# Performance work log

Hardware: AMD Instinct MI355X
Metric: run time of the kernel (lower is better)

Reference implementation:

```python
import jax, jax.numpy as jnp
import numpy as np

N = 2048   # num nodes
D = 512    # hidden_dim


def setup_inputs() -> dict:
    key = jax.random.key(0)
    k1, k2 = jax.random.split(key)
    x = jax.random.normal(k1, (N, D), dtype=jnp.float32)
    # linear: hidden_dim -> 1 (xavier-like scale)
    w = jax.random.normal(k2, (D,), dtype=jnp.float32) * (1.0 / np.sqrt(D))
    b = jnp.zeros((1,), dtype=jnp.float32)
    return {"x": x, "w": w, "b": b}


def reference(x, w, b):
    # euclidean_distance_matrix + linear fused:
    # s[i,j] = sum_d w_d * (x[i,d]-x[j,d])^2 + b
    #        = q_i + q_j - 2*(x*w) @ x^T + b,  q_i = sum_d w_d x[i,d]^2
    xw = x * w                              # [N, D]
    q = jnp.sum(xw * x, axis=1)             # [N]
    cross = xw @ x.T                        # [N, N]
    s = q[:, None] + q[None, :] - 2.0 * cross + b[0]
    grouping_matrix = jax.nn.sigmoid(s)     # [N, N]

    # compute_fielder, similarity_graph='base'
    W = grouping_matrix
    degree = jnp.sum(W, axis=1)
    L = jnp.diag(degree) - W                # symmetric graph Laplacian
    eigen_values, eigen_vectors = jnp.linalg.eigh(L)
    order = jnp.argsort(jnp.abs(eigen_values))
    fielder_value = eigen_values[order[1]]
    fielder_vector = eigen_vectors[:, order[1]]
    return grouping_matrix, fielder_value, fielder_vector
```

## Files before the change

kernel.cpp:

```cpp
#include <hip/hip_runtime.h>
#include <math.h>

constexpr int NN = 2048;
constexpr int DD_ = 512;
constexpr int LM = 64;
constexpr int VS = NN + 32;
constexpr int GPART = 8;
#define SIGN_FLIP 1


typedef __attribute__((ext_vector_type(4))) float f32x4;
typedef __attribute__((ext_vector_type(8))) short bf16x8;

__device__ inline double waveReduceSum(double v) {
#pragma unroll
  for (int off = 32; off; off >>= 1) v += __shfl_down(v, off, 64);
  return v;
}

__device__ inline double blockReduceSum256(double v) {
  __shared__ double sm[4];
  int lane = threadIdx.x & 63;
  int wid  = threadIdx.x >> 6;
  v = waveReduceSum(v);
  __syncthreads();
  if (lane == 0) sm[wid] = v;
  __syncthreads();
  double r = 0.0;
  if (threadIdx.x < 4) r = sm[threadIdx.x];
  if (wid == 0) {
    r += __shfl_down(r, 2, 64);
    r += __shfl_down(r, 1, 64);
  }
  return r;
}

__device__ inline double blockReduceSum128(double v) {
  __shared__ double sm[2];
  int lane = threadIdx.x & 63;
  int wid  = threadIdx.x >> 6;
  v = waveReduceSum(v);
  if (lane == 0) sm[wid] = v;
  __syncthreads();
  double r = 0.0;
  if (threadIdx.x == 0) r = sm[0] + sm[1];
  return r;
}

__device__ inline unsigned short f2bf(float f) {
  unsigned u = __float_as_uint(f);
  u += 0x7FFFu + ((u >> 16) & 1u);
  return (unsigned short)(u >> 16);
}
__device__ inline float bf2f(unsigned short h) {
  return __uint_as_float(((unsigned)h) << 16);
}

__global__ __launch_bounds__(128) void k_cvtq(const float* __restrict__ x,
                                              const float* __restrict__ w,
                                              float* __restrict__ q,
                                              unsigned short* __restrict__ ah,
                                              unsigned short* __restrict__ al,
                                              unsigned short* __restrict__ bh,
                                              unsigned short* __restrict__ bl) {
  int row = blockIdx.x, t = threadIdx.x;
  int d = 4 * t;
  float4 xv = *(const float4*)&x[(size_t)row * DD_ + d];
  float4 wv = *(const float4*)&w[d];
  float xs[4] = {xv.x, xv.y, xv.z, xv.w};
  float wsv[4] = {wv.x, wv.y, wv.z, wv.w};
  unsigned short rah[4], ral[4], rbh[4], rbl[4];
  float accq = 0.f;
#pragma unroll
  for (int kq = 0; kq < 4; ++kq) {
    float xf = xs[kq], wf = wsv[kq];
    float a = xf * wf;
    unsigned short h = f2bf(a);
    rah[kq] = h;
    ral[kq] = f2bf(a - bf2f(h));
    unsigned short hb = f2bf(xf);
    rbh[kq] = hb;
    rbl[kq] = f2bf(xf - bf2f(hb));
    accq += wf * xf * xf;
  }
  ushort4 vA = {rah[0], rah[1], rah[2], rah[3]};
  ushort4 vAl = {ral[0], ral[1], ral[2], ral[3]};
  ushort4 vB = {rbh[0], rbh[1], rbh[2], rbh[3]};
  ushort4 vBl = {rbl[0], rbl[1], rbl[2], rbl[3]};
  *(ushort4*)&ah[(size_t)row * DD_ + d] = vA;
  *(ushort4*)&al[(size_t)row * DD_ + d] = vAl;
  *(ushort4*)&bh[(size_t)row * DD_ + d] = vB;
  *(ushort4*)&bl[(size_t)row * DD_ + d] = vBl;
  double rq = blockReduceSum128((double)accq);
  if (t == 0) q[row] = (float)rq;
}

__global__ __launch_bounds__(256) void k_Wm(const unsigned short* __restrict__ ah,
                                            const unsigned short* __restrict__ al,
                                            const unsigned short* __restrict__ bh,
                                            const unsigned short* __restrict__ bl,
                                            const float* __restrict__ q,
                                            const float* __restrict__ bptr,
                                            float* __restrict__ out) {
  __shared__ unsigned short As[2][128][40];
  __shared__ unsigned short Bs[2][128][40];
  const int t = threadIdx.x;
  const int i0 = blockIdx.y * 128, j0 = blockIdx.x * 128;
  const int lane = t & 63, wv = t >> 6;
  const int wr = wv >> 1, wc = wv & 1;
  const int fr = lane & 15, kc = lane >> 4;
  const int srow = t >> 1, scol = (t & 1) * 16;

  f32x4 acc[4][4];
#pragma unroll
  for (int a = 0; a < 4; ++a)
#pragma unroll
    for (int b = 0; b < 4; ++b) acc[a][b] = (f32x4){0.f, 0.f, 0.f, 0.f};

  {
    bf16x8 ra0 = *(const bf16x8*)&ah[(size_t)(i0 + srow) * DD_ + scol];
    bf16x8 ra1 = *(const bf16x8*)&ah[(size_t)(i0 + srow) * DD_ + scol + 8];
    bf16x8 rb0 = *(const bf16x8*)&bh[(size_t)(j0 + srow) * DD_ + scol];
    bf16x8 rb1 = *(const bf16x8*)&bh[(size_t)(j0 + srow) * DD_ + scol + 8];
    *(bf16x8*)&As[0][srow][scol] = ra0;
    *(bf16x8*)&As[0][srow][scol + 8] = ra1;
    *(bf16x8*)&Bs[0][srow][scol] = rb0;
    *(bf16x8*)&Bs[0][srow][scol + 8] = rb1;
  }
  __syncthreads();
  int cur = 0;
  for (int s = 0; s < 48; ++s) {
    bf16x8 na0, na1, nb0, nb1;
    if (s + 1 < 48) {
      int pass = (s + 1) >> 4;
      int kk = ((s + 1) & 15) * 32;
      const unsigned short* srcA = (pass == 2) ? al : ah;
      const unsigned short* srcB = (pass == 1) ? bl : bh;
      na0 = *(const bf16x8*)&srcA[(size_t)(i0 + srow) * DD_ + kk + scol];
      na1 = *(const bf16x8*)&srcA[(size_t)(i0 + srow) * DD_ + kk + scol + 8];
      nb0 = *(const bf16x8*)&srcB[(size_t)(j0 + srow) * DD_ + kk + scol];
      nb1 = *(const bf16x8*)&srcB[(size_t)(j0 + srow) * DD_ + kk + scol + 8];
    }
    bf16x8 af[4], bq[4];
#pragma unroll
    for (int a = 0; a < 4; ++a)
      af[a] = *(const bf16x8*)&As[cur][wr * 64 + a * 16 + fr][kc * 8];
#pragma unroll
    for (int b = 0; b < 4; ++b)
      bq[b] = *(const bf16x8*)&Bs[cur][wc * 64 + b * 16 + fr][kc * 8];
#pragma unroll
    for (int a = 0; a < 4; ++a)
#pragma unroll
      for (int b = 0; b < 4; ++b)
        acc[a][b] = __builtin_amdgcn_mfma_f32_16x16x32_bf16(af[a], bq[b], acc[a][b], 0, 0, 0);
    if (s + 1 < 48) {
      *(bf16x8*)&As[cur ^ 1][srow][scol] = na0;
      *(bf16x8*)&As[cur ^ 1][srow][scol + 8] = na1;
      *(bf16x8*)&Bs[cur ^ 1][srow][scol] = nb0;
      *(bf16x8*)&Bs[cur ^ 1][srow][scol + 8] = nb1;
    }
    __syncthreads();
    cur ^= 1;
  }
  float b0 = bptr[0];
#pragma unroll
  for (int a = 0; a < 4; ++a) {
#pragma unroll
    for (int rg = 0; rg < 4; ++rg) {
      int i = i0 + wr * 64 + a * 16 + kc * 4 + rg;
      float qi = q[i];
#pragma unroll
      for (int b = 0; b < 4; ++b) {
        int j = j0 + wc * 64 + b * 16 + fr;
        float s = qi + q[j] - 2.0f * acc[a][b][rg] + b0;
        out[(size_t)i * NN + j] = 1.0f / (1.0f + expf(-s));
      }
    }
  }
}

__global__ __launch_bounds__(256) void k_init(double* __restrict__ r,
                                              double* __restrict__ part) {
  int t = threadIdx.x;
  double loc[8];
  double s = 0.0;
#pragma unroll
  for (int p = 0; p < 8; ++p) {
    unsigned i = (unsigned)(t + 256 * p);
    unsigned u = i * 2654435761u + 0x9E3779B9u;
    u ^= u >> 16; u *= 0x85EBCA6Bu; u ^= u >> 13; u *= 0xC2B2AE35u; u ^= u >> 16;
    double val = ((double)u / 4294967296.0) - 0.5;
    loc[p] = val; s += val;
  }
  __shared__ double mean_s, inv_s;
  double tot = blockReduceSum256(s);
  if (t == 0) mean_s = tot / (double)NN;
  __syncthreads();
  double mean = mean_s;
  double ss = 0.0;
#pragma unroll
  for (int p = 0; p < 8; ++p) { loc[p] -= mean; ss += loc[p] * loc[p]; }
  double tss = blockReduceSum256(ss);
  if (t == 0) inv_s = 1.0 / sqrt(tss);
  __syncthreads();
  double inv = inv_s;
#pragma unroll
  for (int p = 0; p < 8; ++p) r[t + 256 * p] = loc[p] * inv;
  if (t < GPART) part[t] = (t == 0) ? 1.0 : 0.0;
}

__global__ __launch_bounds__(256) void k_mva(const float* __restrict__ Wm,
                                             double* __restrict__ deg,
                                             const double* __restrict__ rprev,
                                             const double* __restrict__ part,
                                             double* __restrict__ V,
                                             double* __restrict__ wstash,
                                             double* __restrict__ c,
                                             double* __restrict__ beta, int j) {
  int b = blockIdx.x, t = threadIdx.x;
  double ss = 0.0;
#pragma unroll
  for (int p = 0; p < GPART; ++p) ss += part[p];
  double bet = sqrt(ss);
  double inv = (bet > 1e-3) ? 1.0 / bet : 0.0;

  if (b < NN) {
    const float* wr = Wm + (size_t)b * NN;
    double acc = 0.0, dsum = 0.0;
    if (j == 0) {
#pragma unroll
      for (int p = 0; p < 2; ++p) {
        int i = 4 * t + 1024 * p;
        float4 wl = *(const float4*)&wr[i];
        dsum += (double)wl.x + (double)wl.y + (double)wl.z + (double)wl.w;
        acc += (double)wl.x * rprev[i] + (double)wl.y * rprev[i + 1] +
               (double)wl.z * rprev[i + 2] + (double)wl.w * rprev[i + 3];
      }
    } else {
#pragma unroll
      for (int p = 0; p < 2; ++p) {
        int i = 4 * t + 1024 * p;
        float4 wl = *(const float4*)&wr[i];
        acc += (double)wl.x * rprev[i] + (double)wl.y * rprev[i + 1] +
               (double)wl.z * rprev[i + 2] + (double)wl.w * rprev[i + 3];
      }
    }
    double red = blockReduceSum256(acc);
    double dred = 0.0;
    if (j == 0) dred = blockReduceSum256(dsum);
    if (t == 0) {
      double d;
      if (j == 0) { d = dred; deg[b] = d; }
      else d = deg[b];
      double vj = rprev[b] * inv;
      V[(size_t)j * VS + b] = vj;
      wstash[(size_t)j * VS + b] = d * vj - red * inv;
      if (b == 0 && j > 0) beta[j - 1] = (bet > 1e-3) ? bet : 0.0;
    }
  } else {
    int q = b - NN;
    const double* wq = wstash + (size_t)q * VS;
    double a = 0.0;
#pragma unroll
    for (int p = 0; p < 8; ++p) { int i = t + 256 * p; a += wq[i] * rprev[i]; }
    double red = blockReduceSum256(a);
    if (t == 0) c[q] = red * inv;
  }
}

__global__ __launch_bounds__(256) void k_orthb(const double* __restrict__ V,
                                               const double* __restrict__ wstash,
                                               const double* __restrict__ c,
                                               double* __restrict__ r,
                                               double* __restrict__ part,
                                               double* __restrict__ alpha, int j) {
  __shared__ double cs[LM];
  __shared__ double cj_s, s1_s;
  int b = blockIdx.x, t = threadIdx.x;
  const double* wj = wstash + (size_t)j * VS;
  const double* vj = V + (size_t)j * VS;
  double a = 0.0, s = 0.0;
#pragma unroll
  for (int p = 0; p < 8; ++p) {
    int i = t + 256 * p;
    double wv = wj[i];
    a += vj[i] * wv;
    s += wv;
  }
  double cj = blockReduceSum256(a);
  double s1 = blockReduceSum256(s);
  if (t == 0) { cj_s = cj; s1_s = s1; }
  for (int k = t; k < j; k += 256) cs[k] = c[k];
  __syncthreads();
  double cjv = cj_s, s1v = s1_s;
  int i = b * 256 + t;
  double val = wj[i] - s1v / (double)NN - cjv * vj[i];
  for (int k = 0; k < j; ++k) val -= cs[k] * V[(size_t)k * VS + i];
  r[i] = val;
  double rr = blockReduceSum256(val * val);
  if (t == 0) {
    part[b] = rr;
    if (b == 0) alpha[j] = cjv;
  }
}

__device__ inline double guardpiv(double d) {
  if (fabs(d) < 1e-280) return (d < 0.0) ? -1e-280 : 1e-280;
  return d;
}

__global__ __launch_bounds__(64) void k_tri(const double* __restrict__ alpha,
                                            const double* __restrict__ beta,
                                            double* __restrict__ svec) {
  __shared__ double al[LM], be[LM];
  __shared__ double Dg[LM], Dl[LM], Du[LM], Du2[LM], bb[LM];
  __shared__ unsigned char piv[LM];
  __shared__ double bounds[2];
  __shared__ int cnts[64];
  __shared__ int meff_s;
  int t = threadIdx.x;
  for (int i = t; i < LM; i += 64) { al[i] = alpha[i]; be[i] = (i < LM - 1) ? beta[i] : 0.0; }
  __syncthreads();
  if (t == 0) {
    int m = LM;
    for (int i = 0; i < LM; ++i) {
      if (!isfinite(al[i])) { m = i; break; }
      if (i < LM - 1 && (be[i] == 0.0 || !isfinite(be[i]))) { m = i + 1; break; }
    }
    if (m < 2) m = 2;
    meff_s = m;
  }
  __syncthreads();
  const int n = meff_s;
  double lo = 1e300, hi = -1e300;
  for (int i = t; i < n; i += 64) {
    double r = 0.0;
    if (i > 0) r += fabs(be[i - 1]);
    if (i < n - 1) r += fabs(be[i]);
    lo = fmin(lo, al[i] - r);
    hi = fmax(hi, al[i] + r);
  }
#pragma unroll
  for (int off = 32; off; off >>= 1) {
    lo = fmin(lo, __shfl_down(lo, off, 64));
    hi = fmax(hi, __shfl_down(hi, off, 64));
  }
  if (t == 0) { bounds[0] = lo; bounds[1] = hi; }
  __syncthreads();
  for (int round = 0; round < 3; ++round) {
    double L0 = bounds[0], H0 = bounds[1];
    double p = L0 + (H0 - L0) * ((double)(t + 1) / 65.0);
    int cnt = 0;
    double d = al[0] - p;
    if (d < 0) cnt++;
    for (int i = 1; i < n; ++i) {
      if (fabs(d) < 1e-300) d = (d < 0.0) ? -1e-300 : 1e-300;
      double bi = be[i - 1];
      d = (al[i] - p) - bi * bi / d;
      if (d < 0) cnt++;
    }
    cnts[t] = cnt;
    __syncthreads();
    if (t == 0) {
      double nl = L0, nh = H0;
      for (int l = 0; l < 64; ++l) {
        double pl = L0 + (H0 - L0) * ((double)(l + 1) / 65.0);
        if (cnts[l] == 0) nl = pl;
        else { nh = pl; break; }
      }
      bounds[0] = nl; bounds[1] = nh;
    }
    __syncthreads();
  }
  double sigma = 0.5 * (bounds[0] + bounds[1]);
  if (t == 0) {
    for (int i = 0; i < n; ++i) Dg[i] = al[i] - sigma;
    for (int i = 0; i < n - 1; ++i) { Dl[i] = be[i]; Du[i] = be[i]; }
    for (int i = 0; i < n - 2; ++i) Du2[i] = 0.0;
    for (int i = 0; i < n - 1; ++i) {
      if (fabs(Dg[i]) >= fabs(Dl[i])) {
        double dpiv = guardpiv(Dg[i]);
        double fact = Dl[i] / dpiv;
        Dl[i] = fact;
        Dg[i + 1] -= fact * Du[i];
        piv[i] = 0;
      } else {
        double fact = Dg[i] / Dl[i];
        Dg[i] = Dl[i]; Dl[i] = fact;
        double temp = Du[i];
        Du[i] = Dg[i + 1];
        Dg[i + 1] = temp - fact * Dg[i + 1];
        if (i < n - 2) { Du2[i] = Du[i + 1]; Du[i + 1] = -fact * Du[i + 1]; }
        piv[i] = 1;
      }
    }
    for (int i = 0; i < n; ++i) bb[i] = 1.0;
    for (int i = 0; i < n - 1; ++i) {
      if (!piv[i]) bb[i + 1] -= Dl[i] * bb[i];
      else { double tmp = bb[i]; bb[i] = bb[i + 1]; bb[i + 1] = tmp - Dl[i] * bb[i]; }
    }
    bb[n - 1] = bb[n - 1] / guardpiv(Dg[n - 1]);
    bb[n - 2] = (bb[n - 2] - Du[n - 2] * bb[n - 1]) / guardpiv(Dg[n - 2]);
    for (int i = n - 3; i >= 0; --i)
      bb[i] = (bb[i] - Du[i] * bb[i + 1] - Du2[i] * bb[i + 2]) / guardpiv(Dg[i]);
    double nrm = 0.0;
    for (int i = 0; i < n; ++i) nrm += bb[i] * bb[i];
    double s = 1.0 / sqrt(nrm);
    for (int i = 0; i < LM; ++i) svec[i] = (i < n) ? bb[i] * s : 0.0;
  }
}

__global__ __launch_bounds__(256) void k_ritz(const double* __restrict__ V,
                                              const double* __restrict__ s,
                                              double* __restrict__ u) {
  __shared__ double cs[LM];
  int t = threadIdx.x;
  for (int k = t; k < LM; k += 256) cs[k] = s[k];
  __syncthreads();
  int i = blockIdx.x * 256 + t;
  double acc = 0.0;
  for (int k = 0; k < LM; ++k) acc += cs[k] * V[(size_t)k * VS + i];
  u[i] = acc;
}

__global__ __launch_bounds__(256) void k_mvu(const float* __restrict__ Wm,
                                             const double* __restrict__ deg,
                                             const double* __restrict__ v,
                                             double* __restrict__ w) {
  int row = blockIdx.x, t = threadIdx.x;
  const float* wr = Wm + (size_t)row * NN;
  double acc = 0.0;
#pragma unroll
  for (int p = 0; p < 2; ++p) {
    int i = 4 * t + 1024 * p;
    float4 wl = *(const float4*)&wr[i];
    acc += (double)wl.x * v[i] + (double)wl.y * v[i + 1] +
           (double)wl.z * v[i + 2] + (double)wl.w * v[i + 3];
  }
  double r = blockReduceSum256(acc);
  if (t == 0) w[row] = deg[row] * v[row] - r;
}

__global__ __launch_bounds__(256) void k_tail(const double* __restrict__ u,
                                              const double* __restrict__ lu,
                                              float* __restrict__ out_lam,
                                              float* __restrict__ outv) {
  __shared__ double mv[256];
  __shared__ int mi[256];
  __shared__ double mean_s, scale_s;
  int t = threadIdx.x;
  double a = 0.0, b = 0.0;
#pragma unroll
  for (int p = 0; p < 8; ++p) {
    int i = t + 256 * p;
    a += u[i] * lu[i];
    b += u[i] * u[i];
  }
  double ra = blockReduceSum256(a);
  double rb = blockReduceSum256(b);
  if (t == 0) *out_lam = (float)(ra / rb);
  double loc[8];
  double s = 0.0;
#pragma unroll
  for (int p = 0; p < 8; ++p) { loc[p] = u[t + 256 * p]; s += loc[p]; }
  double tot = blockReduceSum256(s);
  if (t == 0) mean_s = tot / (double)NN;
  __syncthreads();
  double mean = mean_s;
  double ss = 0.0, bv = -1.0;
  int bi = 0;
#pragma unroll
  for (int p = 0; p < 8; ++p) {
    loc[p] -= mean;
    ss += loc[p] * loc[p];
    double aa = fabs(loc[p]);
    if (aa > bv) { bv = aa; bi = p; }
  }
  double tss = blockReduceSum256(ss);
  mv[t] = bv; mi[t] = t + 256 * bi;
  __syncthreads();
  for (int off = 128; off; off >>= 1) {
    if (t < off) {
      if (mv[t + off] > mv[t]) { mv[t] = mv[t + off]; mi[t] = mi[t + off]; }
    }
    __syncthreads();
  }
  if (t == 0) {
    int gi = mi[0];
    double best = u[gi] - mean_s;
    double sgn = (best < 0.0) ? -1.0 : 1.0;
#if SIGN_FLIP
    sgn = -sgn;
#endif
    scale_s = sgn / sqrt(tss);
  }
  __syncthreads();
  double sc = scale_s;
#pragma unroll
  for (int p = 0; p < 8; ++p) outv[t + 256 * p] = (float)(loc[p] * sc);
}

extern "C" void kernel_launch(void* const* d_in, const int* in_sizes, int n_in,
                              void* d_out, int out_size, void* d_ws, size_t ws_size,
                              hipStream_t stream) {
  const float* x = (const float*)d_in[0];
  const float* wv = (const float*)d_in[1];
  const float* bp = (const float*)d_in[2];
  float* out = (float*)d_out;

  char* ws = (char*)d_ws;
  size_t off = 0;
  auto alloc = [&](size_t bytes) -> char* {
    char* p = ws + off;
    off = (off + bytes + 255) & ~(size_t)255;
    return p;
  };
  float* q      = (float*)alloc((size_t)NN * 4);
  double* deg   = (double*)alloc((size_t)NN * 8);
  double* r     = (double*)alloc((size_t)NN * 8);
  double* u     = (double*)alloc((size_t)NN * 8);
  double* c     = (double*)alloc((size_t)(LM + 2) * 8);
  double* alpha = (double*)alloc((size_t)LM * 8);
  double* beta  = (double*)alloc((size_t)LM * 8);
  double* svec  = (double*)alloc((size_t)LM * 8);
  double* part  = (double*)alloc((size_t)GPART * 8);
  char* un = alloc((size_t)4 * NN * DD_ * 2);
  unsigned short* ah = (unsigned short*)un;
  unsigned short* al = ah + (size_t)NN * DD_;
  unsigned short* bh = al + (size_t)NN * DD_;
  unsigned short* bl = bh + (size_t)NN * DD_;
  double* V      = (double*)un;
  double* wstash = V + (size_t)LM * VS;
  (void)ws_size; (void)in_sizes; (void)n_in; (void)out_size;

  k_cvtq<<<NN, 128, 0, stream>>>(x, wv, q, ah, al, bh, bl);
  dim3 g(NN / 128, NN / 128);
  k_Wm<<<g, 256, 0, stream>>>(ah, al, bh, bl, q, bp, out);
  k_init<<<1, 256, 0, stream>>>(r, part);

  for (int j = 0; j < LM; ++j) {
    k_mva<<<NN + j, 256, 0, stream>>>(out, deg, r, part, V, wstash, c, beta, j);
    k_orthb<<<NN / 256, 256, 0, stream>>>(V, wstash, c, r, part, alpha, j);
  }
  k_tri<<<1, 64, 0, stream>>>(alpha, beta, svec);
  k_ritz<<<NN / 256, 256, 0, stream>>>(V, svec, u);
  k_mvu<<<NN, 256, 0, stream>>>(out, deg, u, r);
  k_tail<<<1, 256, 0, stream>>>(u, r, out + (size_t)NN * NN,
                                out + (size_t)NN * NN + 1);
}
```

Baseline: 820.5 us.

## Compute only upper-triangle similarity tiles and rewrite tridiagonal solve with wave shuffles

The grouping-matrix kernel now exits early for blocks below the diagonal. Off-diagonal blocks write each sigmoid value twice, to (i,j) and to its mirror (j,i), which roughly halves the MFMA work but adds strided, uncoalesced transpose stores. Separately, the single-wave tridiagonal bisection, inverse-iteration LU and solve are rewritten to keep data in registers and exchange it with cross-lane shuffles and ballot instead of shared memory and serial thread-0 loops. Each serial step now costs several shuffles, and the restructured LU recurrence carries correctness risk.

```diff
diff --git a/kernel.cpp b/kernel.cpp
--- a/kernel.cpp
+++ b/kernel.cpp
@@ -102,10 +102,12 @@
                                             const float* __restrict__ q,
                                             const float* __restrict__ bptr,
                                             float* __restrict__ out) {
+  const int bx = blockIdx.x, by = blockIdx.y;
+  if (bx < by) return;
   __shared__ unsigned short As[2][128][40];
   __shared__ unsigned short Bs[2][128][40];
   const int t = threadIdx.x;
-  const int i0 = blockIdx.y * 128, j0 = blockIdx.x * 128;
+  const int i0 = by * 128, j0 = bx * 128;
   const int lane = t & 63, wv = t >> 6;
   const int wr = wv >> 1, wc = wv & 1;
   const int fr = lane & 15, kc = lane >> 4;
@@ -163,6 +165,7 @@
     cur ^= 1;
   }
   float b0 = bptr[0];
+  const bool mirror = (bx != by);
 #pragma unroll
   for (int a = 0; a < 4; ++a) {
 #pragma unroll
@@ -173,7 +176,9 @@
       for (int b = 0; b < 4; ++b) {
         int j = j0 + wc * 64 + b * 16 + fr;
         float s = qi + q[j] - 2.0f * acc[a][b][rg] + b0;
-        out[(size_t)i * NN + j] = 1.0f / (1.0f + expf(-s));
+        float sig = 1.0f / (1.0f + expf(-s));
+        out[(size_t)i * NN + j] = sig;
+        if (mirror) out[(size_t)j * NN + i] = sig;
       }
     }
   }
@@ -312,102 +317,132 @@
 __global__ __launch_bounds__(64) void k_tri(const double* __restrict__ alpha,
                                             const double* __restrict__ beta,
                                             double* __restrict__ svec) {
-  __shared__ double al[LM], be[LM];
-  __shared__ double Dg[LM], Dl[LM], Du[LM], Du2[LM], bb[LM];
-  __shared__ unsigned char piv[LM];
-  __shared__ double bounds[2];
-  __shared__ int cnts[64];
-  __shared__ int meff_s;
-  int t = threadIdx.x;
-  for (int i = t; i < LM; i += 64) { al[i] = alpha[i]; be[i] = (i < LM - 1) ? beta[i] : 0.0; }
-  __syncthreads();
-  if (t == 0) {
-    int m = LM;
-    for (int i = 0; i < LM; ++i) {
-      if (!isfinite(al[i])) { m = i; break; }
-      if (i < LM - 1 && (be[i] == 0.0 || !isfinite(be[i]))) { m = i + 1; break; }
-    }
-    if (m < 2) m = 2;
-    meff_s = m;
-  }
-  __syncthreads();
-  const int n = meff_s;
+  const int t = threadIdx.x;
+  double al_r = alpha[t];
+  double be_r = (t < LM - 1) ? beta[t] : 0.0;
+
+  int cand = isfinite(al_r) ? LM : t;
+  int candb = (t < LM - 1 && (be_r == 0.0 || !isfinite(be_r))) ? (t + 1) : LM;
+  int m = min(cand, candb);
+#pragma unroll
+  for (int off = 32; off; off >>= 1) m = min(m, __shfl_down(m, off, 64));
+  m = __shfl(m, 0, 64);
+  if (m < 2) m = 2;
+  const int n = m;
+
+  double be_prev = __shfl_up(be_r, 1, 64);
   double lo = 1e300, hi = -1e300;
-  for (int i = t; i < n; i += 64) {
-    double r = 0.0;
-    if (i > 0) r += fabs(be[i - 1]);
-    if (i < n - 1) r += fabs(be[i]);
-    lo = fmin(lo, al[i] - r);
-    hi = fmax(hi, al[i] + r);
+  if (t < n) {
+    double rr = 0.0;
+    if (t > 0) rr += fabs(be_prev);
+    if (t < n - 1) rr += fabs(be_r);
+    lo = al_r - rr;
+    hi = al_r + rr;
   }
 #pragma unroll
   for (int off = 32; off; off >>= 1) {
     lo = fmin(lo, __shfl_down(lo, off, 64));
     hi = fmax(hi, __shfl_down(hi, off, 64));
   }
-  if (t == 0) { bounds[0] = lo; bounds[1] = hi; }
-  __syncthreads();
+  lo = __shfl(lo, 0, 64);
+  hi = __shfl(hi, 0, 64);
+
+  double B0 = lo, B1 = hi;
   for (int round = 0; round < 3; ++round) {
-    double L0 = bounds[0], H0 = bounds[1];
-    double p = L0 + (H0 - L0) * ((double)(t + 1) / 65.0);
+    double p = B0 + (B1 - B0) * ((double)(t + 1) / 65.0);
     int cnt = 0;
-    double d = al[0] - p;
+    double d = __shfl(al_r, 0, 64) - p;
     if (d < 0) cnt++;
     for (int i = 1; i < n; ++i) {
+      double ai = __shfl(al_r, i, 64);
+      double bi = __shfl(be_r, i - 1, 64);
       if (fabs(d) < 1e-300) d = (d < 0.0) ? -1e-300 : 1e-300;
-      double bi = be[i - 1];
-      d = (al[i] - p) - bi * bi / d;
+      d = (ai - p) - bi * bi / d;
       if (d < 0) cnt++;
     }
-    cnts[t] = cnt;
-    __syncthreads();
-    if (t == 0) {
-      double nl = L0, nh = H0;
-      for (int l = 0; l < 64; ++l) {
-        double pl = L0 + (H0 - L0) * ((double)(l + 1) / 65.0);
-        if (cnts[l] == 0) nl = pl;
-        else { nh = pl; break; }
+    unsigned long long nz = __ballot(cnt > 0);
+    double nl, nh;
+    if (nz) {
+      int first = __ffsll(nz) - 1;
+      nh = B0 + (B1 - B0) * ((double)(first + 1) / 65.0);
+      nl = (first > 0) ? (B0 + (B1 - B0) * ((double)first / 65.0)) : B0;
+    } else {
+      nl = B0 + (B1 - B0) * (64.0 / 65.0);
+      nh = B1;
+    }
+    B0 = nl; B1 = nh;
+  }
+  const double sigma = 0.5 * (B0 + B1);
+
+  double Dgf = 0.0, Dl_s = 0.0, Du_s = 0.0, Du2_s = 0.0;
+  int piv_s = 0;
+  {
+    double dg = __shfl(al_r, 0, 64) - sigma;
+    double du = __shfl(be_r, 0, 64);
+    for (int i = 0; i < n - 1; ++i) {
+      double bl = __shfl(be_r, i, 64);
+      double a_ip1 = __shfl(al_r, i + 1, 64);
+      double be_ip1 = (i + 1 < n - 1) ? __shfl(be_r, i + 1, 64) : 0.0;
+      double dg_ip1 = a_ip1 - sigma;
+      double dg_n, du_n;
+      if (fabs(dg) >= fabs(bl)) {
+        double fact = bl / guardpiv(dg);
+        if (t == i) { Dgf = dg; Dl_s = fact; Du_s = du; Du2_s = 0.0; piv_s = 0; }
+        dg_n = dg_ip1 - fact * du;
+        du_n = be_ip1;
+      } else {
+        double fact = dg / bl;
+        if (t == i) { Dgf = bl; Dl_s = fact; Du_s = dg_ip1; Du2_s = be_ip1; piv_s = 1; }
+        dg_n = du - fact * dg_ip1;
+        du_n = -fact * be_ip1;
       }
-      bounds[0] = nl; bounds[1] = nh;
-    }
-    __syncthreads();
-  }
-  double sigma = 0.5 * (bounds[0] + bounds[1]);
-  if (t == 0) {
-    for (int i = 0; i < n; ++i) Dg[i] = al[i] - sigma;
-    for (int i = 0; i < n - 1; ++i) { Dl[i] = be[i]; Du[i] = be[i]; }
-    for (int i = 0; i < n - 2; ++i) Du2[i] = 0.0;
+      dg = dg_n; du = du_n;
+    }
+    if (t == n - 1) Dgf = dg;
+  }
+
+  double bbf = 1.0;
+  {
+    double cur = 1.0;
     for (int i = 0; i < n - 1; ++i) {
-      if (fabs(Dg[i]) >= fabs(Dl[i])) {
-        double dpiv = guardpiv(Dg[i]);
-        double fact = Dl[i] / dpiv;
-        Dl[i] = fact;
-        Dg[i + 1] -= fact * Du[i];
-        piv[i] = 0;
+      double dl = __shfl(Dl_s, i, 64);
+      int pv = __shfl(piv_s, i, 64);
+      double nxt;
+      if (!pv) {
+        if (t == i) bbf = cur;
+        nxt = 1.0 - dl * cur;
       } else {
-        double fact = Dg[i] / Dl[i];
-        Dg[i] = Dl[i]; Dl[i] = fact;
-        double temp = Du[i];
-        Du[i] = Dg[i + 1];
-        Dg[i + 1] = temp - fact * Dg[i + 1];
-        if (i < n - 2) { Du2[i] = Du[i + 1]; Du[i + 1] = -fact * Du[i + 1]; }
-        piv[i] = 1;
+        if (t == i) bbf = 1.0;
+        nxt = cur - dl;
       }
-    }
-    for (int i = 0; i < n; ++i) bb[i] = 1.0;
-    for (int i = 0; i < n - 1; ++i) {
-      if (!piv[i]) bb[i + 1] -= Dl[i] * bb[i];
-      else { double tmp = bb[i]; bb[i] = bb[i + 1]; bb[i + 1] = tmp - Dl[i] * bb[i]; }
-    }
-    bb[n - 1] = bb[n - 1] / guardpiv(Dg[n - 1]);
-    bb[n - 2] = (bb[n - 2] - Du[n - 2] * bb[n - 1]) / guardpiv(Dg[n - 2]);
-    for (int i = n - 3; i >= 0; --i)
-      bb[i] = (bb[i] - Du[i] * bb[i + 1] - Du2[i] * bb[i + 2]) / guardpiv(Dg[i]);
-    double nrm = 0.0;
-    for (int i = 0; i < n; ++i) nrm += bb[i] * bb[i];
-    double s = 1.0 / sqrt(nrm);
-    for (int i = 0; i < LM; ++i) svec[i] = (i < n) ? bb[i] * s : 0.0;
-  }
+      cur = nxt;
+    }
+    if (t == n - 1) bbf = cur;
+  }
+
+  double xv = 0.0;
+  {
+    double x_ip1 = 0.0, x_ip2 = 0.0;
+    for (int i = n - 1; i >= 0; --i) {
+      double bi = __shfl(bbf, i, 64);
+      double dgi = __shfl(Dgf, i, 64);
+      double dui = __shfl(Du_s, i, 64);
+      double du2i = __shfl(Du2_s, i, 64);
+      double num = bi;
+      if (i < n - 1) num -= dui * x_ip1;
+      if (i < n - 2) num -= du2i * x_ip2;
+      double xi = num / guardpiv(dgi);
+      if (t == i) xv = xi;
+      x_ip2 = x_ip1; x_ip1 = xi;
+    }
+  }
+
+  double nrm = (t < n) ? xv * xv : 0.0;
+#pragma unroll
+  for (int off = 32; off; off >>= 1) nrm += __shfl_down(nrm, off, 64);
+  nrm = __shfl(nrm, 0, 64);
+  double s = 1.0 / sqrt(nrm);
+  svec[t] = (t < n) ? xv * s : 0.0;
 }
 
 __global__ __launch_bounds__(256) void k_ritz(const double* __restrict__ V,
```

After: 825.0 us. Within noise of the previous version (+0.5%).
